# Kernel tuning notes

Hardware: AMD Instinct MI355X
Metric: run time of the kernel (lower is better)

## Reference

```python
import jax, jax.numpy as jnp
import numpy as np

# SSD Detect post-processing constants (match init_kwargs)
NUM_CLASSES = 21
TOP_K = 200
CONF_THRESH = 0.95
NMS_THRESH = 0.45
M_CAND = 600      # candidate cap; chosen so all boxes passing CONF_THRESH fit (~437 expected)
NEG = -1e30


def setup_inputs() -> dict:
    key = jax.random.key(0)
    k1, k2, k3 = jax.random.split(key, 3)
    B, P, C = 8, 8732, NUM_CLASSES
    loc_data = jax.random.normal(k1, (B, P, 4), dtype=jnp.float32)
    conf_data = jax.random.uniform(k2, (B, P, C), dtype=jnp.float32)
    prior_data = jax.random.uniform(k3, (1, P, 4), dtype=jnp.float32)
    return {"loc_data": loc_data, "conf_data": conf_data, "prior_data": prior_data}


def _nms_lane(boxes_all, scores):
    """One (batch, class) lane. boxes_all: [P,4], scores: [P]. Returns [TOP_K, 5]."""
    pass_mask = scores > CONF_THRESH                       # [P]
    masked = jnp.where(pass_mask, scores, jnp.float32(NEG))
    vals, idx = jax.lax.top_k(masked, M_CAND)              # score-desc candidates (prior idx)
    valid = vals > jnp.float32(NEG / 2)                    # passed threshold
    cb = boxes_all[idx]                                    # [M,4] (x1,y1,x2,y2)
    x1, y1, x2, y2 = cb[:, 0], cb[:, 1], cb[:, 2], cb[:, 3]
    area = (x2 - x1) * (y2 - y1)                           # torchvision-style, no clamp
    xx1 = jnp.maximum(x1[:, None], x1[None, :])
    yy1 = jnp.maximum(y1[:, None], y1[None, :])
    xx2 = jnp.minimum(x2[:, None], x2[None, :])
    yy2 = jnp.minimum(y2[:, None], y2[None, :])
    inter = jnp.clip(xx2 - xx1, 0.0) * jnp.clip(yy2 - yy1, 0.0)
    iou = inter / (area[:, None] + area[None, :] - inter)  # [M,M]
    ar = jnp.arange(M_CAND)

    def body(i, supp):
        keep_i = valid[i] & jnp.logical_not(supp[i])
        return supp | (keep_i & (iou[i] > NMS_THRESH) & (ar > i))

    supp = jax.lax.fori_loop(0, M_CAND, body, jnp.zeros((M_CAND,), bool))
    keep = valid & jnp.logical_not(supp)
    order = jnp.argsort(jnp.logical_not(keep))             # stable: kept first, score order
    n = jnp.minimum(keep.sum(), TOP_K)                     # number of kept boxes (<= TOP_K)
    sel_prior = idx[order[:TOP_K]]                         # prior ids of kept (score order)
    slot_valid = jnp.arange(TOP_K) < n
    fp = jnp.argmax(pass_mask)                             # first prior passing threshold
    prior_ids = jnp.where(slot_valid, sel_prior, fp)       # pad with boxes[0] like torch
    out_scores = jnp.where(slot_valid, scores[prior_ids], 0.0)
    out = jnp.concatenate([out_scores[:, None], boxes_all[prior_ids]], axis=1)  # [K,5]
    return jnp.where(pass_mask.any(), out, jnp.zeros_like(out))


def _forward(loc_data, conf_data, prior_data):
    # prior_data is accepted per the torch signature but unused by the forward math.
    per_batch = jax.vmap(
        lambda boxes, conf_b: jax.vmap(lambda s: _nms_lane(boxes, s))(conf_b[:, 1:].T)
    )
    out_fg = per_batch(loc_data, conf_data)                # [B, C-1, K, 5]
    bg = jnp.zeros_like(out_fg[:, :1])                     # background class row stays 0
    return jnp.concatenate([bg, out_fg], axis=1)           # [B, C, K, 5]


def reference(loc_data, conf_data, prior_data):
    return _forward(loc_data, conf_data, prior_data)
```

## Files before the change

kernel.cpp:

```cpp
#include <hip/hip_runtime.h>
#include <float.h>
#include <math.h>


#define P_PRIORS  8732
#define C_CLASSES 21
#define B_BATCH   8
#define TOPK      200
#define MCAND     600
#define CONF_T    0.95f
#define NMS_T     0.45f
#define NB        64
#define MINB      0x3F733334u

__device__ __forceinline__ uint64_t pack_key(float sc, int p) {
    return ((uint64_t)__float_as_uint(sc) << 32) | (uint32_t)(~(uint32_t)p);
}
__device__ __forceinline__ int bucket_of(uint64_t key) {
    unsigned d = (unsigned)(key >> 32) - MINB;
    int b = (int)(d >> 14);
    return b < (NB - 1) ? b : (NB - 1);
}

#define IOU_ROW(BI, AI, MW, DIAG) do {                                   \
    float xx1 = fmaxf((BI).x, bj.x);                                     \
    float yy1 = fmaxf((BI).y, bj.y);                                     \
    float xx2 = fminf((BI).z, bj.z);                                     \
    float yy2 = fminf((BI).w, bj.w);                                     \
    float ww  = fmaxf(xx2 - xx1, 0.0f);                                  \
    float hh  = fmaxf(yy2 - yy1, 0.0f);                                  \
    float inter = ww * hh;                                               \
    float den   = ((AI) + aj) - inter;              \
    float iou   = inter / den;               \
    uint64_t m = __ballot(iou > NMS_T);                                  \
    if (k == c) m &= (DIAG);                                             \
    (MW) = (lid == k) ? m : (MW);                                        \
} while (0)

__device__ __forceinline__ void iou_chunk(
    int c, int wid, int lid, int M, int kmax,
    const float4* s_jb, const float* s_area, uint64_t* s_bm)
{
    const int i0 = (c << 6) + wid;
    const float4 b0 = s_jb[i0],      b1 = s_jb[i0 + 16],
                 b2 = s_jb[i0 + 32], b3 = s_jb[i0 + 48];
    const float  a0 = s_area[i0],      a1 = s_area[i0 + 16],
                 a2 = s_area[i0 + 32], a3 = s_area[i0 + 48];
    const uint64_t d0 = ~0ull << (wid + 1);
    const uint64_t d1 = ~0ull << (wid + 17);
    const uint64_t d2 = ~0ull << (wid + 33);
    const uint64_t d3 = (wid == 15) ? 0ull : (~0ull << (wid + 49));
    uint64_t w0 = 0, w1 = 0, w2 = 0, w3 = 0;
    for (int k = c; k < kmax; ++k) {
        const float4 bj = s_jb[(k << 6) + lid];
        const float  aj = s_area[(k << 6) + lid];
        IOU_ROW(b0, a0, w0, d0);
        IOU_ROW(b1, a1, w1, d1);
        IOU_ROW(b2, a2, w2, d2);
        IOU_ROW(b3, a3, w3, d3);
    }
    if (lid >= c && lid < kmax) {
        if (i0      < M) s_bm[(size_t)(i0     ) * 10 + lid] = w0;
        if (i0 + 16 < M) s_bm[(size_t)(i0 + 16) * 10 + lid] = w1;
        if (i0 + 32 < M) s_bm[(size_t)(i0 + 32) * 10 + lid] = w2;
        if (i0 + 48 < M) s_bm[(size_t)(i0 + 48) * 10 + lid] = w3;
    }
}

__global__ __launch_bounds__(1024) void detect_one(
    const float* __restrict__ loc, const float* __restrict__ conf,
    float* __restrict__ out)
{
    const int b   = blockIdx.x & 7;
    const int cls = blockIdx.x >> 3;
    const int tid = threadIdx.x;
    float* o = out + ((size_t)(b * C_CLASSES + cls)) * TOPK * 5;

    if (cls == 0) {
        for (int k = tid; k < TOPK * 5; k += 1024) o[k] = 0.0f;
        return;
    }

    const float*  confb = conf + (size_t)b * P_PRIORS * C_CLASSES + cls;
    const float4* loc4  = (const float4*)(loc + (size_t)b * P_PRIORS * 4);

    __shared__ uint64_t s_bm[MCAND * 10];
    __shared__ float4   s_jb[640];
    __shared__ float    s_area[640];
    __shared__ float    s_ssc[MCAND];
    __shared__ int      s_bcnt[NB], s_bcur[NB], s_boff[NB];
    __shared__ int      s_cnt, s_fp;
    __shared__ uint64_t s_suppw[10], s_keepw[10];
    __shared__ int      s_prefix[10], s_n, s_mstop, s_done;

    uint64_t* s_k   = s_bm;
    uint64_t* s_g   = s_bm + 1024;
    uint64_t* s_srt = s_bm + 2048;

    if (tid < NB)                    s_bcnt[tid] = 0;
    else if (tid < 2 * NB)           s_bcur[tid - NB] = 0;
    else if (tid == 2 * NB)        { s_cnt = 0; s_fp = 0x7FFFFFFF; }
    __syncthreads();

    {
        const int lid = tid & 63;
        float vcur  = confb[(size_t)tid * C_CLASSES];
        float vnext = confb[(size_t)(tid + 1024) * C_CLASSES];
        #pragma unroll
        for (int r = 0; r < 9; ++r) {
            float v = vcur;
            vcur = vnext;
            if (r + 2 <= 7) {
                vnext = confb[(size_t)(tid + ((r + 2) << 10)) * C_CLASSES];
            } else if (r + 2 == 8) {
                int pn = tid + 8192;
                vnext = (pn < P_PRIORS) ? confb[(size_t)pn * C_CLASSES] : 0.0f;
            } else {
                vnext = 0.0f;
            }
            int p = tid + (r << 10);
            bool pass = v > CONF_T;
            uint64_t mask = __ballot(pass);
            if (mask != 0) {
                int leader = (int)__ffsll((unsigned long long)mask) - 1;
                int base = 0;
                if (lid == leader) {
                    base = atomicAdd(&s_cnt, __popcll(mask));
                    atomicMin(&s_fp, p);
                }
                base = __shfl(base, leader, 64);
                if (pass) {
                    int pos = base + __popcll(mask & ((1ull << lid) - 1ull));
                    if (pos < 1024) s_k[pos] = pack_key(v, p);
                }
            }
        }
    }
    __syncthreads();
    int cnt = s_cnt; if (cnt > 1024) cnt = 1024;
    if (cnt == 0) {
        for (int k = tid; k < TOPK * 5; k += 1024) o[k] = 0.0f;
        return;
    }

    for (int t = tid; t < cnt; t += 1024)
        atomicAdd(&s_bcnt[bucket_of(s_k[t])], 1);
    __syncthreads();

    if (tid < 64) {
        int c = s_bcnt[63 - tid];
        int incl = c;
        #pragma unroll
        for (int d = 1; d < 64; d <<= 1) {
            int u = __shfl_up(incl, d, 64);
            if (tid >= d) incl += u;
        }
        s_boff[63 - tid] = incl - c;
    }
    __syncthreads();

    for (int t = tid; t < cnt; t += 1024) {
        uint64_t kt = s_k[t];
        int bb = bucket_of(kt);
        s_g[s_boff[bb] + atomicAdd(&s_bcur[bb], 1)] = kt;
    }
    __syncthreads();

    const int M = cnt < MCAND ? cnt : MCAND;
    {
        const int wid = tid >> 6, lid = tid & 63;
        for (int bb = wid; bb < NB; bb += 16) {
            int st = s_boff[bb], n = s_bcnt[bb];
            for (int e = lid; e < n; e += 64) {
                uint64_t kq = s_g[st + e];
                int r = st;
                for (int q = 0; q < n; ++q)
                    r += (s_g[st + q] > kq) ? 1 : 0;
                if (r < MCAND) s_srt[r] = kq;
            }
        }
    }
    __syncthreads();

    for (int i = tid; i < M; i += 1024) {
        uint64_t key = s_srt[i];
        int p = (int)(~(uint32_t)key);
        s_ssc[i]  = __uint_as_float((uint32_t)(key >> 32));
        float4 bx = loc4[p];
        s_jb[i]   = bx;
        s_area[i] = (bx.z - bx.x) * (bx.w - bx.y);
    }
    for (int i = M + tid; i < 640; i += 1024) {
        s_jb[i]   = make_float4(INFINITY, INFINITY, INFINITY, INFINITY);
        s_area[i] = INFINITY;
    }
    const int fp = s_fp;
    __syncthreads();

    const int kmax = (M + 63) >> 6;

    {
        const int wid = tid >> 6, lid = tid & 63;
        const int w   = (lid < 10) ? lid : 0;
        uint64_t supp = 0;
        int kept = 0, mstop = M;
        const int nch = kmax;

        iou_chunk(0, wid, lid, M, kmax, s_jb, s_area, s_bm);
        __syncthreads();

        for (int c = 0; c < nch; ++c) {
            if (wid == 0) {
                const int ibeg = c << 6;
                const int iend = min(ibeg + 64, M);
                uint64_t rb[8];
                #pragma unroll
                for (int d = 0; d < 8; ++d) {
                    int i = ibeg + d;
                    rb[d] = (i < iend) ? s_bm[(size_t)i * 10 + w] : 0;
                }
                for (int i = ibeg; i < iend; ++i) {
                    uint64_t row = rb[i & 7];
                    if (w < c) row = 0;
                    int ip = i + 8;
                    rb[i & 7] = (ip < iend) ? s_bm[(size_t)ip * 10 + w] : 0;
                    bool mybit = (w == c) && ((supp >> (i & 63)) & 1ull);
                    if (!__any((int)mybit)) {
                        supp |= row;
                        if (++kept == TOPK) { mstop = i + 1; break; }
                    }
                }
                if (lid == 0) s_done = (kept >= TOPK) ? 1 : 0;
                if (kept < TOPK && c + 1 < nch)
                    iou_chunk(c + 1, 0, lid, M, kmax, s_jb, s_area, s_bm);
            } else if (c + 1 < nch) {
                iou_chunk(c + 1, wid, lid, M, kmax, s_jb, s_area, s_bm);
            }
            __syncthreads();
            if (s_done) break;
        }
        if (wid == 0) {
            if (lid < 10) s_suppw[lid] = supp;
            if (lid == 0) s_mstop = mstop;
        }
    }
    __syncthreads();

    if (tid == 0) {
        const int Me = s_mstop;
        int total = 0;
        for (int w = 0; w < 10; ++w) {
            uint64_t kw = 0;
            int rem = Me - (w << 6);
            if (rem > 0) {
                uint64_t vm = (rem >= 64) ? ~0ull : ((1ull << rem) - 1ull);
                kw = (~s_suppw[w]) & vm;
            }
            s_keepw[w]  = kw;
            s_prefix[w] = total;
            total += __popcll(kw);
        }
        s_n = total < TOPK ? total : TOPK;
    }
    __syncthreads();

    const int n  = s_n;
    const int Me = s_mstop;
    float4 fbox = loc4[fp];
    for (int k = tid; k < TOPK; k += 1024) {
        if (k >= n) {
            o[k * 5 + 0] = 0.0f;
            o[k * 5 + 1] = fbox.x; o[k * 5 + 2] = fbox.y;
            o[k * 5 + 3] = fbox.z; o[k * 5 + 4] = fbox.w;
        }
    }
    for (int t = tid; t < Me; t += 1024) {
        uint64_t kw = s_keepw[t >> 6];
        if ((kw >> (t & 63)) & 1ull) {
            int r = s_prefix[t >> 6] + __popcll(kw & ((1ull << (t & 63)) - 1ull));
            if (r < TOPK) {
                float4 bx = s_jb[t];
                o[r * 5 + 0] = s_ssc[t];
                o[r * 5 + 1] = bx.x; o[r * 5 + 2] = bx.y;
                o[r * 5 + 3] = bx.z; o[r * 5 + 4] = bx.w;
            }
        }
    }
}

extern "C" void kernel_launch(void* const* d_in, const int* in_sizes, int n_in,
                              void* d_out, int out_size, void* d_ws, size_t ws_size,
                              hipStream_t stream) {
    const float* loc  = (const float*)d_in[0];
    const float* conf = (const float*)d_in[1];
    float* out = (float*)d_out;
    (void)d_ws; (void)ws_size;

    detect_one<<<dim3(B_BATCH * C_CLASSES), dim3(1024), 0, stream>>>(loc, conf, out);
}
```

Before: 109.2 us.

## Cap pipelined NMS to first 320 candidates with full fallback path

```diff
diff --git a/kernel.cpp b/kernel.cpp
--- a/kernel.cpp
+++ b/kernel.cpp
@@ -18,7 +18,7 @@
 }
 __device__ __forceinline__ int bucket_of(uint64_t key) {
     unsigned d = (unsigned)(key >> 32) - MINB;
-    int b = (int)(d >> 14);
+    int b = (int)(d >> 10);
     return b < (NB - 1) ? b : (NB - 1);
 }
 
@@ -38,7 +38,7 @@
 } while (0)
 
 __device__ __forceinline__ void iou_chunk(
-    int c, int wid, int lid, int M, int kmax,
+    int c, int wid, int lid, int M, int kend,
     const float4* s_jb, const float* s_area, uint64_t* s_bm)
 {
     const int i0 = (c << 6) + wid;
@@ -51,7 +51,7 @@
     const uint64_t d2 = ~0ull << (wid + 33);
     const uint64_t d3 = (wid == 15) ? 0ull : (~0ull << (wid + 49));
     uint64_t w0 = 0, w1 = 0, w2 = 0, w3 = 0;
-    for (int k = c; k < kmax; ++k) {
+    for (int k = c; k < kend; ++k) {
         const float4 bj = s_jb[(k << 6) + lid];
         const float  aj = s_area[(k << 6) + lid];
         IOU_ROW(b0, a0, w0, d0);
@@ -59,7 +59,7 @@
         IOU_ROW(b2, a2, w2, d2);
         IOU_ROW(b3, a3, w3, d3);
     }
-    if (lid >= c && lid < kmax) {
+    if (lid >= c && lid < kend) {
         if (i0      < M) s_bm[(size_t)(i0     ) * 10 + lid] = w0;
         if (i0 + 16 < M) s_bm[(size_t)(i0 + 16) * 10 + lid] = w1;
         if (i0 + 32 < M) s_bm[(size_t)(i0 + 32) * 10 + lid] = w2;
@@ -198,15 +198,16 @@
     __syncthreads();
 
     const int kmax = (M + 63) >> 6;
+    const int kcap = kmax < 5 ? kmax : 5;
 
     {
         const int wid = tid >> 6, lid = tid & 63;
         const int w   = (lid < 10) ? lid : 0;
         uint64_t supp = 0;
         int kept = 0, mstop = M;
-        const int nch = kmax;
-
-        iou_chunk(0, wid, lid, M, kmax, s_jb, s_area, s_bm);
+        const int nch = kcap;
+
+        iou_chunk(0, wid, lid, M, kcap, s_jb, s_area, s_bm);
         __syncthreads();
 
         for (int c = 0; c < nch; ++c) {
@@ -232,9 +233,9 @@
                 }
                 if (lid == 0) s_done = (kept >= TOPK) ? 1 : 0;
                 if (kept < TOPK && c + 1 < nch)
-                    iou_chunk(c + 1, 0, lid, M, kmax, s_jb, s_area, s_bm);
+                    iou_chunk(c + 1, 0, lid, M, kcap, s_jb, s_area, s_bm);
             } else if (c + 1 < nch) {
-                iou_chunk(c + 1, wid, lid, M, kmax, s_jb, s_area, s_bm);
+                iou_chunk(c + 1, wid, lid, M, kcap, s_jb, s_area, s_bm);
             }
             __syncthreads();
             if (s_done) break;
@@ -245,6 +246,53 @@
         }
     }
     __syncthreads();
+
+    if (s_done == 0 && M > 320) {
+        const int wid = tid >> 6, lid = tid & 63;
+        for (int i = wid; i < M; i += 16) {
+            float4 bi = s_jb[i];
+            float  ai = s_area[i];
+            const int k0 = i >> 6;
+            uint64_t diag = ((i & 63) == 63) ? 0ull : (~0ull << ((i & 63) + 1));
+            uint64_t myw = 0;
+            for (int k = k0; k < kmax; ++k) {
+                float4 bj = s_jb[(k << 6) + lid];
+                float  aj = s_area[(k << 6) + lid];
+                float xx1 = fmaxf(bi.x, bj.x);
+                float yy1 = fmaxf(bi.y, bj.y);
+                float xx2 = fminf(bi.z, bj.z);
+                float yy2 = fminf(bi.w, bj.w);
+                float ww  = fmaxf(xx2 - xx1, 0.0f);
+                float hh  = fmaxf(yy2 - yy1, 0.0f);
+                float inter = ww * hh;
+                float den   = (ai + aj) - inter;
+                float iou   = inter / den;
+                uint64_t m = __ballot(iou > NMS_T);
+                if (k == k0) m &= diag;
+                myw = (lid == k) ? m : myw;
+            }
+            if (lid >= k0 && lid < kmax) s_bm[(size_t)i * 10 + lid] = myw;
+        }
+        __syncthreads();
+        if (tid < 64) {
+            const int w = (tid < 10) ? tid : 0;
+            uint64_t supp = 0;
+            int kept = 0, ms = M;
+            for (int i = 0; i < M; ++i) {
+                uint64_t row = s_bm[(size_t)i * 10 + w];
+                if (w < (i >> 6)) row = 0;
+                unsigned part  = (unsigned)(supp >> (i & 32));
+                unsigned wordv = (unsigned)__builtin_amdgcn_readlane((int)part, i >> 6);
+                if (!((wordv >> (i & 31)) & 1u)) {
+                    supp |= row;
+                    if (++kept == TOPK) { ms = i + 1; break; }
+                }
+            }
+            if (tid < 10) s_suppw[tid] = supp;
+            if (tid == 0) s_mstop = ms;
+        }
+        __syncthreads();
+    }
 
     if (tid == 0) {
         const int Me = s_mstop;
```

Result: slower. 266.7 us (+144.2%).
